# Kernel tuning notes

Measured on AMD Instinct MI355X. Metric: run time of the kernel, lower is better.

Reference implementation:

```python
import jax, jax.numpy as jnp
import numpy as np

NU, NI, D = 100000, 50000, 64
N = NU + NI            # total graph nodes (users + items)
NNZ = 2_400_000        # edges per adjacency (~avg degree 16)
BRI_START = 50000      # conf.num_bri_user_start


def setup_inputs() -> dict:
    key = jax.random.key(0)
    ks = jax.random.split(key, 32)
    emb = lambda k, n: (0.01 * jax.random.normal(k, (n, D))).astype(jnp.float32)
    inp = {
        'ue': emb(ks[0], NU), 'ie': emb(ks[1], NI),
        'fue': emb(ks[2], NU), 'fie': emb(ks[3], NI),
        'sgu': emb(ks[4], NU), 'sgi': emb(ks[5], NI),
        'igu': emb(ks[6], NU), 'igi': emb(ks[7], NI),
    }
    # 4 sparse adjacency matrices in COO form; values ~ normalized adjacency scale
    for i in range(4):
        inp[f'r{i+1}'] = jax.random.randint(ks[8 + 3 * i], (NNZ,), 0, N, dtype=jnp.int32)
        inp[f'c{i+1}'] = jax.random.randint(ks[9 + 3 * i], (NNZ,), 0, N, dtype=jnp.int32)
        inp[f'v{i+1}'] = (jax.random.uniform(ks[10 + 3 * i], (NNZ,)) * (1.0 / 16)).astype(jnp.float32)
    inp['user'] = jax.random.randint(ks[20], (8192,), 0, NU, dtype=jnp.int32)
    inp['pos'] = jax.random.randint(ks[21], (8192,), 0, NI, dtype=jnp.int32)
    inp['neg'] = jax.random.randint(ks[22], (8192,), 0, NI, dtype=jnp.int32)
    inp['s_bri'] = jax.random.randint(ks[23], (4096,), 0, NU, dtype=jnp.int32)
    inp['i_bri'] = jax.random.randint(ks[24], (4096,), 0, NU, dtype=jnp.int32)
    inp['i_bri_pos'] = jax.random.randint(ks[25], (4096,), 0, NI, dtype=jnp.int32)
    inp['i_bri_neg'] = jax.random.randint(ks[26], (4096,), 0, NI, dtype=jnp.int32)
    return inp


def _spmm(rows, cols, vals, x):
    # COO SpMM: out[r] += v * x[c]
    return jax.ops.segment_sum(vals[:, None] * x[cols], rows, num_segments=N)


def _gcn_layer(rows, cols, vals, user_embed, item_embed):
    # 3-hop propagation with residual; mean over the 4 hop embeddings
    h = jnp.concatenate([user_embed, item_embed], axis=0)  # [N, D]
    acc = h
    for _ in range(3):
        h = _spmm(rows, cols, vals, h) + h
        acc = acc + h
    final = acc * 0.25
    return final[:NU], final[NU:]


def _bce_ones(p):
    return -jnp.mean(jnp.log(p))


def _bce_zeros(p):
    return -jnp.mean(jnp.log1p(-p))


def _forward(ue, ie, fue, fie, sgu, sgi, igu, igi,
             v1, v2, v3, v4,
             r1, c1, r2, c2, r3, c3, r4, c4,
             user, pos, neg, s_bri, i_bri, i_bri_pos, i_bri_neg):
    u_emb, it_emb = _gcn_layer(r1, c1, v1, ue, ie)
    cu_emb, ci_emb = _gcn_layer(r2, c2, v2, fue, fie)
    gsu_emb, _ = _gcn_layer(r3, c3, v3, sgu, sgi)
    giu_emb, gii_emb = _gcn_layer(r4, c4, v4, igu, igi)

    # BPR rating loss + L2
    u_b = u_emb[user]
    ip_b = it_emb[pos]
    in_b = it_emb[neg]
    pos_pred = jnp.sum(u_b * ip_b, axis=1)
    neg_pred = jnp.sum(u_b * in_b, axis=1)
    l2 = 0.01 * (u_b ** 2 + ip_b ** 2 + in_b ** 2).sum(axis=-1)
    rating_loss = -jnp.sum(jax.nn.log_sigmoid(pos_pred - neg_pred)) + jnp.sum(l2)

    # social DGI-style loss (sigmoid applied post-concat == per-part)
    g_soc = jnp.mean(gsu_emb[BRI_START:], axis=0, keepdims=True)       # [1, D]
    g_soc_rep = jnp.broadcast_to(g_soc, (s_bri.shape[0], D))
    soc_real = jax.nn.sigmoid(jnp.concatenate([u_emb[s_bri], g_soc_rep], axis=1))
    soc_fake = jax.nn.sigmoid(jnp.concatenate([cu_emb[s_bri], g_soc_rep], axis=1))
    social_loss = _bce_ones(soc_real) + _bce_zeros(soc_fake)

    # infor DGI-style loss
    g_iu = jnp.mean(jax.nn.sigmoid(giu_emb[i_bri]), axis=0, keepdims=True)       # [1, D]
    g_ii = jnp.mean(jax.nn.sigmoid(gii_emb[i_bri_pos]), axis=0, keepdims=True)   # [1, D]
    g_emb = jnp.broadcast_to(jnp.concatenate([g_iu, g_ii], axis=1), (i_bri.shape[0], 2 * D))
    infor_real = jnp.concatenate([jax.nn.sigmoid(u_emb[i_bri]), g_emb], axis=1)
    infor_fake = jnp.concatenate([jax.nn.sigmoid(cu_emb[i_bri]), g_emb], axis=1)
    infor_loss = _bce_ones(infor_real) + _bce_zeros(infor_fake)

    obj = rating_loss + 100.0 * social_loss + 1000.0 * infor_loss
    return jnp.stack([obj, rating_loss, social_loss, infor_loss])


def reference(ue, ie, fue, fie, sgu, sgi, igu, igi,
              v1, v2, v3, v4,
              r1, c1, r2, c2, r3, c3, r4, c4,
              user, pos, neg, s_bri, i_bri, i_bri_pos, i_bri_neg):
    return _forward(ue, ie, fue, fie, sgu, sgi, igu, igi,
                    v1, v2, v3, v4,
                    r1, c1, r2, c2, r3, c3, r4, c4,
                    user, pos, neg, s_bri, i_bri, i_bri_pos, i_bri_neg)
```

## Files before the change

kernel.cpp:

```cpp
#include <hip/hip_runtime.h>
#include <hip/hip_bf16.h>
#include <stdint.h>

#define NU        100000
#define NI        50000
#define NN        150000
#define D         64
#define NNZ       2400000
#define CAP       48
#define BRI_STARTC 50000
#define NB        8192
#define NS        4096
#define NA        4

#define NPART 8
#define PROWS (NN / NPART)

#define VAL_DEC   (1.f / 262144.f)

#define HSCALE     128.f
#define INV_HSCALE (1.f / 128.f)

typedef int   vint4 __attribute__((ext_vector_type(4)));
typedef float vflt4 __attribute__((ext_vector_type(4)));


__device__ __forceinline__ float logsig(float x) {
    if (x > 0.f) return -log1pf(expf(-x));
    else         return x - log1pf(expf(x));
}

__device__ __forceinline__ float waveReduce(float v) {
    #pragma unroll
    for (int off = 32; off > 0; off >>= 1) v += __shfl_down(v, off, 64);
    return v;
}

__device__ __forceinline__ float fp8dec(unsigned char b) {
    return __builtin_amdgcn_cvt_f32_fp8((unsigned int)b, 0);
}
__device__ __forceinline__ unsigned char fp8enc(float f) {
    return (unsigned char)(__builtin_amdgcn_cvt_pk_fp8_f32(f, f, 0u, false) & 0xFFu);
}

__device__ __forceinline__ float finalRow(const float* __restrict__ ue, const float* __restrict__ ie,
                                          const unsigned char* __restrict__ B1,
                                          const unsigned char* __restrict__ B2,
                                          const unsigned char* __restrict__ B3, int r, int lane) {
    float h0 = (r < NU) ? ue[r * D + lane] : ie[(r - NU) * D + lane];
    size_t o = (size_t)r * D + lane;
    float hs = fp8dec(B1[o]) + fp8dec(B2[o]) + fp8dec(B3[o]);
    return 0.25f * (h0 + hs * INV_HSCALE);
}


struct BuildArgs {
    const int*   rows[NA];
    const int*   cols[NA];
    const float* vals[NA];
    int*          count[NA];
    unsigned int* edges[NA];
};

struct InitArgs {
    const float*   ue[NA];
    const float*   ie[NA];
    unsigned char* H[NA];
};

struct SpmmArgs {
    const unsigned int* Hin[NA];
    unsigned int*       Hout[NA];
    const int*          count[NA];
    const unsigned int* edges[NA];
    const int*          list[NA];
    int rowbase[NA];
    int nrows[NA];
};


__global__ void __launch_bounds__(256) build4_kernel(BuildArgs B) {
    const int a    = blockIdx.y;
    const int p    = blockIdx.x & (NPART - 1);
    const int lo   = p * PROWS;
    const int hi   = lo + PROWS;
    const int sub  = blockIdx.x >> 3;
    const int nsub = gridDim.x >> 3;
    const int t    = sub * blockDim.x + threadIdx.x;
    const int nt   = nsub * blockDim.x;
    const int*   rows = B.rows[a];
    const int*   cols = B.cols[a];
    const float* vals = B.vals[a];
    int*          count = B.count[a];
    unsigned int* edges = B.edges[a];
    for (int e4 = t; e4 < NNZ / 4; e4 += nt) {
        vint4 r4 = __builtin_nontemporal_load((const vint4*)rows + e4);
        vint4 c4 = __builtin_nontemporal_load((const vint4*)cols + e4);
        vflt4 v4 = __builtin_nontemporal_load((const vflt4*)vals + e4);
        #pragma unroll
        for (int k = 0; k < 4; k++) {
            int r = r4[k];
            if (r < lo || r >= hi) continue;
            int pos = atomicAdd(&count[r], 1);
            if (pos < CAP) {
                unsigned int q = (unsigned int)(v4[k] * 262144.f + 0.5f);
                if (q > 16383u) q = 16383u;
                edges[(size_t)r * CAP + pos] = (q << 18) | (unsigned int)c4[k];
            }
        }
    }
}

__global__ void init4_kernel(InitArgs I) {
    const int a = blockIdx.y;
    int idx = blockIdx.x * blockDim.x + threadIdx.x;
    if (idx >= NN * D / 4) return;
    float4 v;
    if (idx < NU * D / 4) v = ((const float4*)I.ue[a])[idx];
    else                  v = ((const float4*)I.ie[a])[idx - NU * D / 4];
    uchar4 o;
    o.x = fp8enc(v.x * HSCALE); o.y = fp8enc(v.y * HSCALE);
    o.z = fp8enc(v.z * HSCALE); o.w = fp8enc(v.w * HSCALE);
    ((uchar4*)I.H[a])[idx] = o;
}

__global__ void mklist_kernel(const int* __restrict__ user, const int* __restrict__ pos,
                              const int* __restrict__ neg, const int* __restrict__ s_bri,
                              const int* __restrict__ i_bri, const int* __restrict__ i_bri_pos,
                              int* __restrict__ L0, int* __restrict__ L1, int* __restrict__ L3) {
    int i = blockIdx.x * blockDim.x + threadIdx.x;
    if (i < 8192)       L0[i] = user[i];
    else if (i < 16384) L0[i] = NU + pos[i - 8192];
    else if (i < 24576) L0[i] = NU + neg[i - 16384];
    else if (i < 28672) L0[i] = s_bri[i - 24576];
    else if (i < 32768) L0[i] = i_bri[i - 28672];
    if (i < 4096)       L1[i] = s_bri[i];
    else if (i < 8192)  L1[i] = i_bri[i - 4096];
    if (i < 4096)       L3[i] = i_bri[i];
    else if (i < 8192)  L3[i] = NU + i_bri_pos[i - 4096];
}

__device__ __forceinline__ void accum4(const unsigned int* __restrict__ Hin4,
                                       uint4 w, int jbase, int cnt, int l16,
                                       float4& acc) {
    unsigned int ww[4] = { w.x, w.y, w.z, w.w };
    unsigned int xw[4];
    #pragma unroll
    for (int e = 0; e < 4; e++)
        xw[e] = Hin4[(int)(ww[e] & 0x3FFFFu) * 16 + l16];
    #pragma unroll
    for (int e = 0; e < 4; e++) {
        bool ok = (jbase + e) < cnt;
        unsigned int x = ok ? xw[e] : 0u;
        float v = ok ? (float)(ww[e] >> 18) * VAL_DEC : 0.f;
        acc.x += v * __builtin_amdgcn_cvt_f32_fp8(x, 0);
        acc.y += v * __builtin_amdgcn_cvt_f32_fp8(x, 1);
        acc.z += v * __builtin_amdgcn_cvt_f32_fp8(x, 2);
        acc.w += v * __builtin_amdgcn_cvt_f32_fp8(x, 3);
    }
}

__global__ void __launch_bounds__(256) spmm2_kernel(SpmmArgs A) {
    const int a     = blockIdx.y;
    const int nrows = A.nrows[a];
    int wave = (blockIdx.x * blockDim.x + threadIdx.x) >> 6;
    if (wave * 2 >= nrows) return;
    const int lane = threadIdx.x & 63;
    const int l16  = lane & 15;
    const int g    = (lane >> 4) & 1;
    int widx = wave * 2 + (lane >> 5);
    if (widx >= nrows) widx = nrows - 1;
    const int* list = A.list[a];
    const int row = list ? list[widx] : (A.rowbase[a] + widx);

    const unsigned int* __restrict__ Hin4 = A.Hin[a];
    unsigned int sw = Hin4[row * 16 + l16];
    int cnt = A.count[a][row];
    const uint4* ep4 = (const uint4*)(A.edges[a] + (size_t)row * CAP);
    uint4 w0 = ep4[g];
    uint4 w1 = ep4[2 + g];
    uint4 w2 = ep4[4 + g];
    uint4 w3 = ep4[6 + g];
    if (cnt > CAP) cnt = CAP;

    float4 acc = make_float4(0.f, 0.f, 0.f, 0.f);
    accum4(Hin4, w0,  4 * g,      cnt, l16, acc);
    accum4(Hin4, w1,  8 + 4 * g,  cnt, l16, acc);
    if (cnt > 16) {
        accum4(Hin4, w2, 16 + 4 * g, cnt, l16, acc);
        accum4(Hin4, w3, 24 + 4 * g, cnt, l16, acc);
    }
    if (cnt > 32) {
        uint4 w4 = ep4[8 + g];
        uint4 w5 = ep4[10 + g];
        accum4(Hin4, w4, 32 + 4 * g, cnt, l16, acc);
        accum4(Hin4, w5, 40 + 4 * g, cnt, l16, acc);
    }

    acc.x += __shfl_xor(acc.x, 16, 64);
    acc.y += __shfl_xor(acc.y, 16, 64);
    acc.z += __shfl_xor(acc.z, 16, 64);
    acc.w += __shfl_xor(acc.w, 16, 64);
    acc.x += __builtin_amdgcn_cvt_f32_fp8(sw, 0);
    acc.y += __builtin_amdgcn_cvt_f32_fp8(sw, 1);
    acc.z += __builtin_amdgcn_cvt_f32_fp8(sw, 2);
    acc.w += __builtin_amdgcn_cvt_f32_fp8(sw, 3);
    if (g == 0) {
        unsigned int lo = __builtin_amdgcn_cvt_pk_fp8_f32(acc.x, acc.y, 0u, false);
        unsigned int hi = __builtin_amdgcn_cvt_pk_fp8_f32(acc.z, acc.w, 0u, false);
        A.Hout[a][row * 16 + l16] = (lo & 0xFFFFu) | (hi << 16);
    }
}

__global__ void rating_kernel(const float* __restrict__ ue, const float* __restrict__ ie,
                              const unsigned char* __restrict__ B1, const unsigned char* __restrict__ B2,
                              const unsigned char* __restrict__ B3,
                              const int* __restrict__ user, const int* __restrict__ pos,
                              const int* __restrict__ neg, float* __restrict__ slot) {
    int wave = (blockIdx.x * blockDim.x + threadIdx.x) >> 6;
    int lane = threadIdx.x & 63;
    if (wave >= NB) return;
    int u = user[wave], p = pos[wave], n = neg[wave];
    float ub  = finalRow(ue, ie, B1, B2, B3, u, lane);
    float ipb = finalRow(ue, ie, B1, B2, B3, NU + p, lane);
    float inb = finalRow(ue, ie, B1, B2, B3, NU + n, lane);
    float pp = waveReduce(ub * ipb);
    float np = waveReduce(ub * inb);
    float l2 = waveReduce(ub * ub + ipb * ipb + inb * inb);
    if (lane == 0) {
        atomicAdd(slot, -logsig(pp - np) + 0.01f * l2);
    }
}

__global__ void sumlog_kernel(const float* __restrict__ ue, const float* __restrict__ ie,
                              const unsigned char* __restrict__ B1, const unsigned char* __restrict__ B2,
                              const unsigned char* __restrict__ B3,
                              const int* __restrict__ idx, int rowbase, int negate,
                              float* __restrict__ slot) {
    int wave = (blockIdx.x * blockDim.x + threadIdx.x) >> 6;
    int lane = threadIdx.x & 63;
    if (wave >= NS) return;
    int r = rowbase + idx[wave];
    float x = finalRow(ue, ie, B1, B2, B3, r, lane);
    float t = logsig(negate ? -x : x);
    float s = waveReduce(t);
    if (lane == 0) atomicAdd(slot, s);
}

__global__ void colsum_range_kernel(const float* __restrict__ ue, const float* __restrict__ ie,
                                    const unsigned char* __restrict__ B1, const unsigned char* __restrict__ B2,
                                    const unsigned char* __restrict__ B3, float* __restrict__ gsum) {
    int wave = (blockIdx.x * blockDim.x + threadIdx.x) >> 6;
    int lane = threadIdx.x & 63;
    int nw = (gridDim.x * blockDim.x) >> 6;
    float s = 0.f;
    for (int r = BRI_STARTC + wave; r < NU; r += nw)
        s += finalRow(ue, ie, B1, B2, B3, r, lane);
    atomicAdd(&gsum[lane], s);
}

__global__ void colsum_sig_kernel(const float* __restrict__ ue, const float* __restrict__ ie,
                                  const unsigned char* __restrict__ B1, const unsigned char* __restrict__ B2,
                                  const unsigned char* __restrict__ B3,
                                  const int* __restrict__ idx, int rowbase,
                                  float* __restrict__ gsum) {
    int wave = (blockIdx.x * blockDim.x + threadIdx.x) >> 6;
    int lane = threadIdx.x & 63;
    int nw = (gridDim.x * blockDim.x) >> 6;
    float s = 0.f;
    for (int i = wave; i < NS; i += nw) {
        int r = rowbase + idx[i];
        float x = finalRow(ue, ie, B1, B2, B3, r, lane);
        s += 1.f / (1.f + expf(-x));
    }
    atomicAdd(&gsum[lane], s);
}

__global__ void final_kernel(const float* __restrict__ scal, float* __restrict__ out) {
    int lane = threadIdx.x;
    float gs  = scal[8 + lane] * (1.f / 50000.f);
    float sp  = waveReduce(logsig(gs));
    float sn  = waveReduce(logsig(-gs));
    float giu = scal[72 + lane] * (1.f / 4096.f);
    float gup = waveReduce(logf(giu));
    float gun = waveReduce(log1pf(-giu));
    float gii = scal[136 + lane] * (1.f / 4096.f);
    float gip = waveReduce(logf(gii));
    float gin = waveReduce(log1pf(-gii));
    if (lane == 0) {
        float rating = scal[0];
        float social = (-(scal[1]) - 4096.f * sp) / 524288.f
                     + (-(scal[2]) - 4096.f * sn) / 524288.f;
        float infor  = (-(scal[3]) - 4096.f * (gup + gip)) / 786432.f
                     + (-(scal[4]) - 4096.f * (gun + gin)) / 786432.f;
        float obj = rating + 100.f * social + 1000.f * infor;
        out[0] = obj; out[1] = rating; out[2] = social; out[3] = infor;
    }
}


extern "C" void kernel_launch(void* const* d_in, const int* in_sizes, int n_in,
                              void* d_out, int out_size, void* d_ws, size_t ws_size,
                              hipStream_t stream) {
    const float* uembs[NA] = { (const float*)d_in[0], (const float*)d_in[2],
                               (const float*)d_in[4], (const float*)d_in[6] };
    const float* iembs[NA] = { (const float*)d_in[1], (const float*)d_in[3],
                               (const float*)d_in[5], (const float*)d_in[7] };
    const int*   rA[NA]; const int* cA[NA]; const float* vA[NA];
    for (int a = 0; a < NA; a++) {
        rA[a] = (const int*)d_in[8 + 3 * a];
        cA[a] = (const int*)d_in[9 + 3 * a];
        vA[a] = (const float*)d_in[10 + 3 * a];
    }
    const int* user      = (const int*)d_in[20];
    const int* pos       = (const int*)d_in[21];
    const int* neg       = (const int*)d_in[22];
    const int* s_bri     = (const int*)d_in[23];
    const int* i_bri     = (const int*)d_in[24];
    const int* i_bri_pos = (const int*)d_in[25];

    const size_t SZBUF  = (size_t)NN * D;
    const size_t EDGESZ = (size_t)NN * CAP * sizeof(unsigned int);
    const size_t CNTSZ  = (size_t)NN * sizeof(int);
    const size_t LISTSZ = (size_t)(32768 + 8192 + 8192) * sizeof(int);
    const size_t need_merged = 12 * SZBUF + NA * EDGESZ + NA * CNTSZ + 1024 + LISTSZ;
    char* ws = (char*)d_ws;

    if (ws_size >= need_merged) {
        auto P = [&](int a, int h) -> unsigned char* {
            return (unsigned char*)(ws + (size_t)(3 * a + h) * SZBUF);
        };
        unsigned int* EDG[NA]; int* CNT[NA];
        char* edgbase = ws + 12 * SZBUF;
        char* cntbase = edgbase + NA * EDGESZ;
        for (int a = 0; a < NA; a++) {
            EDG[a] = (unsigned int*)(edgbase + (size_t)a * EDGESZ);
            CNT[a] = (int*)(cntbase + (size_t)a * CNTSZ);
        }
        float* SCAL  = (float*)(cntbase + NA * CNTSZ);
        int*   LIST0 = (int*)((char*)SCAL + 1024);
        int*   LIST1 = LIST0 + 32768;
        int*   LIST3 = LIST1 + 8192;

        hipMemsetAsync(SCAL, 0, 256 * sizeof(float), stream);
        hipMemsetAsync(cntbase, 0, NA * CNTSZ, stream);
        mklist_kernel<<<128, 256, 0, stream>>>(user, pos, neg, s_bri, i_bri, i_bri_pos,
                                               LIST0, LIST1, LIST3);

        BuildArgs B;
        InitArgs  I;
        for (int a = 0; a < NA; a++) {
            B.rows[a] = rA[a]; B.cols[a] = cA[a]; B.vals[a] = vA[a];
            B.count[a] = CNT[a]; B.edges[a] = EDG[a];
            I.ue[a] = uembs[a]; I.ie[a] = iembs[a]; I.H[a] = P(a, 0);
        }
        build4_kernel<<<dim3(2048, NA), 256, 0, stream>>>(B);
        init4_kernel<<<dim3(NN * D / 4 / 256, NA), 256, 0, stream>>>(I);

        SpmmArgs H1, H2, H3;
        const int* l3[NA]   = { LIST0, LIST1, nullptr, LIST3 };
        const int  rb3[NA]  = { 0, 0, 50000, 0 };
        const int  nr3[NA]  = { 32768, 8192, 50000, 8192 };
        for (int a = 0; a < NA; a++) {
            H1.Hin[a] = (const unsigned int*)P(a, 0); H1.Hout[a] = (unsigned int*)P(a, 1);
            H2.Hin[a] = (const unsigned int*)P(a, 1); H2.Hout[a] = (unsigned int*)P(a, 2);
            H3.Hin[a] = (const unsigned int*)P(a, 2); H3.Hout[a] = (unsigned int*)P(a, 0);
            H1.count[a] = H2.count[a] = H3.count[a] = CNT[a];
            H1.edges[a] = H2.edges[a] = H3.edges[a] = EDG[a];
            H1.list[a] = H2.list[a] = nullptr; H3.list[a] = l3[a];
            H1.rowbase[a] = H2.rowbase[a] = 0;  H3.rowbase[a] = rb3[a];
            H1.nrows[a] = H2.nrows[a] = NN;     H3.nrows[a] = nr3[a];
        }
        spmm2_kernel<<<dim3((NN + 7) / 8, NA), 256, 0, stream>>>(H1);
        spmm2_kernel<<<dim3((NN + 7) / 8, NA), 256, 0, stream>>>(H2);
        spmm2_kernel<<<dim3((50000 + 7) / 8, NA), 256, 0, stream>>>(H3);

        rating_kernel<<<NB * 64 / 256, 256, 0, stream>>>(uembs[0], iembs[0], P(0,1), P(0,2), P(0,0),
                                                         user, pos, neg, &SCAL[0]);
        sumlog_kernel<<<NS * 64 / 256, 256, 0, stream>>>(uembs[0], iembs[0], P(0,1), P(0,2), P(0,0),
                                                         s_bri, 0, 0, &SCAL[1]);
        sumlog_kernel<<<NS * 64 / 256, 256, 0, stream>>>(uembs[0], iembs[0], P(0,1), P(0,2), P(0,0),
                                                         i_bri, 0, 0, &SCAL[3]);
        sumlog_kernel<<<NS * 64 / 256, 256, 0, stream>>>(uembs[1], iembs[1], P(1,1), P(1,2), P(1,0),
                                                         s_bri, 0, 1, &SCAL[2]);
        sumlog_kernel<<<NS * 64 / 256, 256, 0, stream>>>(uembs[1], iembs[1], P(1,1), P(1,2), P(1,0),
                                                         i_bri, 0, 1, &SCAL[4]);
        colsum_range_kernel<<<256, 256, 0, stream>>>(uembs[2], iembs[2], P(2,1), P(2,2), P(2,0),
                                                     &SCAL[8]);
        colsum_sig_kernel<<<64, 256, 0, stream>>>(uembs[3], iembs[3], P(3,1), P(3,2), P(3,0),
                                                  i_bri, 0, &SCAL[72]);
        colsum_sig_kernel<<<64, 256, 0, stream>>>(uembs[3], iembs[3], P(3,1), P(3,2), P(3,0),
                                                  i_bri_pos, NU, &SCAL[136]);
        final_kernel<<<1, 64, 0, stream>>>(SCAL, (float*)d_out);
        return;
    }

    unsigned char* P0 = (unsigned char*)(ws);
    unsigned char* P1 = (unsigned char*)(ws + SZBUF);
    unsigned char* P2 = (unsigned char*)(ws + 2 * SZBUF);
    unsigned int* EDGES = (unsigned int*)(ws + 3 * SZBUF);
    int*   COUNT = (int*)  (ws + 3 * SZBUF + EDGESZ);
    float* SCAL  = (float*)(ws + 3 * SZBUF + EDGESZ + CNTSZ);
    int*   LIST0 = (int*)  (ws + 3 * SZBUF + EDGESZ + CNTSZ + 1024);
    int*   LIST1 = LIST0 + 32768;
    int*   LIST3 = LIST1 + 8192;

    hipMemsetAsync(SCAL, 0, 256 * sizeof(float), stream);
    mklist_kernel<<<128, 256, 0, stream>>>(user, pos, neg, s_bri, i_bri, i_bri_pos,
                                           LIST0, LIST1, LIST3);

    const int* lists[NA] = { LIST0, LIST1, (const int*)nullptr, LIST3 };
    const int  nlist[NA] = { 32768, 8192, 50000, 8192 };
    const int  lbase[NA] = { 0, 0, 50000, 0 };

    for (int a = 0; a < NA; a++) {
        hipMemsetAsync(COUNT, 0, CNTSZ, stream);
        BuildArgs B{};
        B.rows[0] = rA[a]; B.cols[0] = cA[a]; B.vals[0] = vA[a];
        B.count[0] = COUNT; B.edges[0] = EDGES;
        build4_kernel<<<dim3(2048, 1), 256, 0, stream>>>(B);
        InitArgs I{};
        I.ue[0] = uembs[a]; I.ie[0] = iembs[a]; I.H[0] = P0;
        init4_kernel<<<dim3(NN * D / 4 / 256, 1), 256, 0, stream>>>(I);

        auto mkspmm = [&](unsigned char* in, unsigned char* out, const int* list,
                          int rowbase, int nrows) {
            SpmmArgs S{};
            S.Hin[0] = (const unsigned int*)in; S.Hout[0] = (unsigned int*)out;
            S.count[0] = COUNT; S.edges[0] = EDGES;
            S.list[0] = list; S.rowbase[0] = rowbase; S.nrows[0] = nrows;
            spmm2_kernel<<<dim3((nrows + 7) / 8, 1), 256, 0, stream>>>(S);
        };
        mkspmm(P0, P1, nullptr, 0, NN);
        mkspmm(P1, P2, nullptr, 0, NN);
        mkspmm(P2, P0, lists[a], lbase[a], nlist[a]);

        const float* ue = uembs[a]; const float* ie = iembs[a];
        if (a == 0) {
            rating_kernel<<<NB * 64 / 256, 256, 0, stream>>>(ue, ie, P1, P2, P0, user, pos, neg, &SCAL[0]);
            sumlog_kernel<<<NS * 64 / 256, 256, 0, stream>>>(ue, ie, P1, P2, P0, s_bri, 0, 0, &SCAL[1]);
            sumlog_kernel<<<NS * 64 / 256, 256, 0, stream>>>(ue, ie, P1, P2, P0, i_bri, 0, 0, &SCAL[3]);
        } else if (a == 1) {
            sumlog_kernel<<<NS * 64 / 256, 256, 0, stream>>>(ue, ie, P1, P2, P0, s_bri, 0, 1, &SCAL[2]);
            sumlog_kernel<<<NS * 64 / 256, 256, 0, stream>>>(ue, ie, P1, P2, P0, i_bri, 0, 1, &SCAL[4]);
        } else if (a == 2) {
            colsum_range_kernel<<<256, 256, 0, stream>>>(ue, ie, P1, P2, P0, &SCAL[8]);
        } else {
            colsum_sig_kernel<<<64, 256, 0, stream>>>(ue, ie, P1, P2, P0, i_bri, 0, &SCAL[72]);
            colsum_sig_kernel<<<64, 256, 0, stream>>>(ue, ie, P1, P2, P0, i_bri_pos, NU, &SCAL[136]);
        }
    }

    final_kernel<<<1, 64, 0, stream>>>(SCAL, (float*)d_out);
}
```

Baseline: 1.400 ms.

## Replace global-atomic ELL build with two-pass LDS bucket sort

The old build read every COO edge once per row partition and appended it to the row-major ELL table with global atomic counters. It is replaced by two kernels. The first bins each edge segment into 256-row buckets in shared memory and writes bucket offset tables. The second gathers each bucket's edges from all segments into LDS slots and writes dense edge rows and counts. This removes the scattered global atomics and repeated input passes, but adds an intermediate 8-byte-per-edge buffer, reusing the hop buffers. The second kernel's per-thread serial gather loops also give it limited parallelism.

```diff
diff --git a/kernel.cpp b/kernel.cpp
--- a/kernel.cpp
+++ b/kernel.cpp
@@ -13,6 +13,11 @@
 #define NS        4096
 #define NA        4
 
+#define NSEG   512
+#define SEGLEN 4688
+#define BROWS  256
+#define NBKT   586
+
 #define NPART 8
 #define PROWS (NN / NPART)
 
@@ -53,6 +58,21 @@
     return 0.25f * (h0 + hs * INV_HSCALE);
 }
 
+
+struct SortArgs {
+    const int*   rows[NA];
+    const int*   cols[NA];
+    const float* vals[NA];
+    uint2*       abuf[NA];
+    int*         tab[NA];
+};
+
+struct ScatArgs {
+    const uint2* abuf[NA];
+    const int*   tab[NA];
+    unsigned int* edges[NA];
+    int*          count[NA];
+};
 
 struct BuildArgs {
     const int*   rows[NA];
@@ -78,6 +98,79 @@
     int nrows[NA];
 };
 
+
+__global__ void __launch_bounds__(256) binA_kernel(SortArgs S) {
+    __shared__ uint2 stage[SEGLEN];
+    __shared__ int   hist[NBKT + 1];
+    __shared__ int   base[NBKT + 1];
+    const int a  = blockIdx.y;
+    const int b  = blockIdx.x;
+    const int t  = threadIdx.x;
+    const int e0 = b * SEGLEN;
+    const int n  = min(SEGLEN, NNZ - e0);
+    for (int k = t; k < NBKT + 1; k += 256) hist[k] = 0;
+    __syncthreads();
+    const int n4 = n >> 2;
+    for (int i4 = t; i4 < n4; i4 += 256) {
+        vint4 r4 = __builtin_nontemporal_load((const vint4*)(S.rows[a] + e0) + i4);
+        vint4 c4 = __builtin_nontemporal_load((const vint4*)(S.cols[a] + e0) + i4);
+        vflt4 v4 = __builtin_nontemporal_load((const vflt4*)(S.vals[a] + e0) + i4);
+        #pragma unroll
+        for (int kk = 0; kk < 4; kk++) {
+            int r = r4[kk];
+            unsigned int q = (unsigned int)(v4[kk] * 262144.f + 0.5f);
+            if (q > 16383u) q = 16383u;
+            stage[i4 * 4 + kk] = make_uint2((q << 18) | (unsigned int)c4[kk], (unsigned int)r);
+            atomicAdd(&hist[r >> 8], 1);
+        }
+    }
+    __syncthreads();
+    if (t == 0) {
+        int run = 0;
+        for (int k = 0; k < NBKT; k++) { base[k] = run; run += hist[k]; }
+        base[NBKT] = run;
+    }
+    __syncthreads();
+    int* tb = S.tab[a] + (size_t)b * (NBKT + 1);
+    for (int k = t; k < NBKT + 1; k += 256) tb[k] = base[k];
+    __syncthreads();
+    for (int i = t; i < n; i += 256) {
+        int k = (int)(stage[i].y >> 8);
+        int p = atomicAdd(&base[k], 1);
+        S.abuf[a][e0 + p] = stage[i];
+    }
+}
+
+__global__ void __launch_bounds__(256) binB_kernel(ScatArgs S) {
+    __shared__ unsigned int slots[BROWS * CAP];
+    __shared__ int cnt[BROWS];
+    const int a    = blockIdx.y;
+    const int k    = blockIdx.x;
+    const int t    = threadIdx.x;
+    const int rlo  = k * BROWS;
+    const int rcnt = min(BROWS, NN - rlo);
+    cnt[t] = 0;
+    __syncthreads();
+    const int*   tab = S.tab[a];
+    const uint2* ab  = S.abuf[a];
+    for (int b = t; b < NSEG; b += 256) {
+        const int* tb = tab + (size_t)b * (NBKT + 1);
+        int lo = tb[k];
+        int hi = tb[k + 1];
+        int e0 = b * SEGLEN;
+        for (int j = lo; j < hi; j++) {
+            uint2 ed = ab[e0 + j];
+            int rl = (int)(ed.y & 255u);
+            int p = atomicAdd(&cnt[rl], 1);
+            if (p < CAP) slots[rl * CAP + p] = ed.x;
+        }
+    }
+    __syncthreads();
+    unsigned int* eg = S.edges[a] + (size_t)rlo * CAP;
+    for (int i = t; i < rcnt * CAP; i += 256)
+        eg[i] = slots[i];
+    if (t < rcnt) S.count[a][rlo + t] = cnt[t];
+}
 
 __global__ void __launch_bounds__(256) build4_kernel(BuildArgs B) {
     const int a    = blockIdx.y;
@@ -98,14 +191,14 @@
         vint4 c4 = __builtin_nontemporal_load((const vint4*)cols + e4);
         vflt4 v4 = __builtin_nontemporal_load((const vflt4*)vals + e4);
         #pragma unroll
-        for (int k = 0; k < 4; k++) {
-            int r = r4[k];
+        for (int kk = 0; kk < 4; kk++) {
+            int r = r4[kk];
             if (r < lo || r >= hi) continue;
             int pos = atomicAdd(&count[r], 1);
             if (pos < CAP) {
-                unsigned int q = (unsigned int)(v4[k] * 262144.f + 0.5f);
+                unsigned int q = (unsigned int)(v4[kk] * 262144.f + 0.5f);
                 if (q > 16383u) q = 16383u;
-                edges[(size_t)r * CAP + pos] = (q << 18) | (unsigned int)c4[k];
+                edges[(size_t)r * CAP + pos] = (q << 18) | (unsigned int)c4[kk];
             }
         }
     }
@@ -323,7 +416,9 @@
     const size_t EDGESZ = (size_t)NN * CAP * sizeof(unsigned int);
     const size_t CNTSZ  = (size_t)NN * sizeof(int);
     const size_t LISTSZ = (size_t)(32768 + 8192 + 8192) * sizeof(int);
-    const size_t need_merged = 12 * SZBUF + NA * EDGESZ + NA * CNTSZ + 1024 + LISTSZ;
+    const size_t TABSZ  = (size_t)NSEG * (NBKT + 1) * sizeof(int);
+    const size_t need_merged = 12 * SZBUF + NA * EDGESZ + NA * CNTSZ + 1024 + LISTSZ
+                             + NA * TABSZ;
     char* ws = (char*)d_ws;
 
     if (ws_size >= need_merged) {
@@ -341,20 +436,29 @@
         int*   LIST0 = (int*)((char*)SCAL + 1024);
         int*   LIST1 = LIST0 + 32768;
         int*   LIST3 = LIST1 + 8192;
+        char*  tabbase = (char*)(LIST3 + 8192);
 
         hipMemsetAsync(SCAL, 0, 256 * sizeof(float), stream);
-        hipMemsetAsync(cntbase, 0, NA * CNTSZ, stream);
         mklist_kernel<<<128, 256, 0, stream>>>(user, pos, neg, s_bri, i_bri, i_bri_pos,
                                                LIST0, LIST1, LIST3);
 
-        BuildArgs B;
-        InitArgs  I;
+        SortArgs SA; ScatArgs SB;
         for (int a = 0; a < NA; a++) {
-            B.rows[a] = rA[a]; B.cols[a] = cA[a]; B.vals[a] = vA[a];
-            B.count[a] = CNT[a]; B.edges[a] = EDG[a];
+            SA.rows[a] = rA[a]; SA.cols[a] = cA[a]; SA.vals[a] = vA[a];
+            SA.abuf[a] = (uint2*)P(a, 1);
+            SA.tab[a]  = (int*)(tabbase + (size_t)a * TABSZ);
+            SB.abuf[a] = (const uint2*)P(a, 1);
+            SB.tab[a]  = SA.tab[a];
+            SB.edges[a] = EDG[a];
+            SB.count[a] = CNT[a];
+        }
+        binA_kernel<<<dim3(NSEG, NA), 256, 0, stream>>>(SA);
+        binB_kernel<<<dim3(NBKT, NA), 256, 0, stream>>>(SB);
+
+        InitArgs I;
+        for (int a = 0; a < NA; a++) {
             I.ue[a] = uembs[a]; I.ie[a] = iembs[a]; I.H[a] = P(a, 0);
         }
-        build4_kernel<<<dim3(2048, NA), 256, 0, stream>>>(B);
         init4_kernel<<<dim3(NN * D / 4 / 256, NA), 256, 0, stream>>>(I);
 
         SpmmArgs H1, H2, H3;
```

After: 1.214 ms. -13.3%, faster.
